# Kernel tuning notes

Hardware: AMD Instinct MI355X
Metric: run time of the kernel (lower is better)

Reference implementation:

```python
import jax, jax.numpy as jnp
import numpy as np

BN_EPS = 1e-5


def gcn_conv(x, src, dst, W, b):
    # PyG GCNConv: add self-loops, symmetric normalization, bias after aggregation
    n = x.shape[0]
    h = x @ W                                   # [N, d]
    deg = jnp.zeros((n,), x.dtype).at[dst].add(1.0) + 1.0  # in-degree + self-loop
    dinv = jax.lax.rsqrt(deg)
    norm = dinv[src] * dinv[dst]                # [E]
    agg = jnp.zeros_like(h).at[dst].add(h[src] * norm[:, None])
    agg = agg + h * (dinv * dinv)[:, None]      # self-loop messages
    return agg + b


def batchnorm(x, gamma, beta):
    mu = x.mean(0)
    var = x.var(0)  # biased, as torch BN training mode
    return (x - mu) * jax.lax.rsqrt(var + BN_EPS) * gamma + beta


def mha(x, w_in, b_in, w_out, b_out, n_heads=4):
    # torch nn.MultiheadAttention, input [L, N, E]
    L, N, d = x.shape
    hd = d // n_heads
    qkv = x @ w_in.T + b_in                     # [L, N, 3d]
    q, k, v = jnp.split(qkv, 3, axis=-1)
    rh = lambda t: t.reshape(L, N, n_heads, hd)
    q = rh(q) * (1.0 / np.sqrt(hd))
    k, v = rh(k), rh(v)
    scores = jnp.einsum('lnhd,mnhd->nhlm', q, k)
    a = jax.nn.softmax(scores, axis=-1)
    o = jnp.einsum('nhlm,mnhd->lnhd', a, v).reshape(L, N, d)
    return o @ w_out.T + b_out


def setup_inputs() -> dict:
    key = jax.random.key(0)
    N, d, E, L, R = 50000, 128, 400000, 3, 4
    ks = jax.random.split(key, 12)
    s = 1.0 / np.sqrt(d)
    return {
        'features': jax.random.normal(ks[0], (N, d), jnp.float32),
        'rel_emb': jax.random.normal(ks[1], (R, d), jnp.float32),
        'edge_index': jax.random.randint(ks[2], (R, 2, E), 0, N, dtype=jnp.int32),
        'W_gcn': jax.random.normal(ks[3], (L, d, d), jnp.float32) * s,
        'b_gcn': jnp.zeros((L, d), jnp.float32),
        'bn_gamma': jnp.ones((L - 1, d), jnp.float32),
        'bn_beta': jnp.zeros((L - 1, d), jnp.float32),
        'W_rt': jax.random.normal(ks[4], (L, d, d), jnp.float32) * s,
        'b_rt': jnp.zeros((L, d), jnp.float32),
        'attn_w_in': jax.random.normal(ks[5], (3 * d, d), jnp.float32) * s,
        'attn_b_in': jnp.zeros((3 * d,), jnp.float32),
        'attn_w_out': jax.random.normal(ks[6], (d, d), jnp.float32) * s,
        'attn_b_out': jnp.zeros((d,), jnp.float32),
        'alphas': jnp.full((4,), 0.95, jnp.float32),
        'fusion_q': jax.random.normal(ks[7], (d,), jnp.float32),
        'fusion_w': jax.random.normal(ks[8], (d, d), jnp.float32) * s,
        'fusion_b': jnp.zeros((d,), jnp.float32),
    }


def reference(features, rel_emb, edge_index, W_gcn, b_gcn, bn_gamma, bn_beta,
              W_rt, b_rt, attn_w_in, attn_b_in, attn_w_out, attn_b_out,
              alphas, fusion_q, fusion_w, fusion_b):
    L = W_gcn.shape[0]
    # RelationGCN unpacks rel_emb as (poi_r, s_r, d_r, n_r) and processes
    # relations in order (n, poi, s, d) -> permute to processing order.
    perm = jnp.array([3, 0, 1, 2])
    rels = rel_emb[perm]                # [4, d], order (n, poi, s, d)
    edges = edge_index[perm]            # [4, 2, E]
    embs = jnp.broadcast_to(features, (4,) + features.shape)  # all start at features

    def inner(emb, r, src, dst, Wg, bg, gamma, beta):
        h = gcn_conv(emb * r, src, dst, Wg, bg)
        return emb + jax.nn.leaky_relu(batchnorm(h, gamma, beta))

    for i in range(L - 1):
        embs = jax.vmap(inner, in_axes=(0, 0, 0, 0, None, None, None, None))(
            embs, rels, edges[:, 0], edges[:, 1],
            W_gcn[i], b_gcn[i], bn_gamma[i], bn_beta[i])
        rels = rels @ W_rt[i].T + b_rt[i]
        # dropout p=0.0 -> identity

    embs = jax.vmap(lambda e, r, s_, t_: gcn_conv(e * r, s_, t_, W_gcn[-1], b_gcn[-1]))(
        embs, rels, edges[:, 0], edges[:, 1])
    rels = rels @ W_rt[-1].T + b_rt[-1]

    # PM_Model mis-unpacks RelationGCN outputs (returned order n,poi,s,d as
    # poi,s,d,n). CrossLayer then stacks (n_emb, poi_emb, d_emb, s_emb) which in
    # true processing order is (d, n, s, poi):
    stk = jnp.stack([embs[3], embs[0], embs[2], embs[1]])  # [4, N, d]
    fusion = mha(stk, attn_w_in, attn_b_in, attn_w_out, attn_b_out)
    a = alphas  # [alpha_n, alpha_poi, alpha_d, alpha_s]
    n_f = fusion[0] * a[0] + (1 - a[0]) * stk[0]
    poi_f = fusion[1] * a[1] + (1 - a[1]) * stk[1]
    d_f = fusion[2] * a[2] + (1 - a[2]) * stk[2]
    s_f = fusion[3] * a[3] + (1 - a[3]) * stk[3]

    def score(f):
        return jnp.mean(jnp.sum(jax.nn.leaky_relu(f @ fusion_w.T + fusion_b) * fusion_q, axis=1))

    w = jax.nn.softmax(jnp.stack([score(n_f), score(poi_f), score(s_f), score(d_f)]))
    region = w[0] * n_f + w[1] * poi_f + w[2] * s_f + w[3] * d_f

    # Final multiplies use the same mis-unpacked rel names:
    # n_r<-rels[3](true d), poi_r<-rels[0](true n), s_r<-rels[1], d_r<-rels[2]
    return (region, region * rels[3], region * rels[0], region * rels[1], region * rels[2])
```

## Files before the change

### kernel.cpp

```cpp
#include <hip/hip_runtime.h>
#include <cstdio>

#define DD 128
#define NREL 4

using short8 = __attribute__((ext_vector_type(8))) short;
using f32x4  = __attribute__((ext_vector_type(4))) float;

struct PtrB4 { const unsigned short* p[4]; };
struct OutB4 { unsigned short* p[4]; };

__device__ __forceinline__ int edge_perm(int r) { return (r + 3) & 3; }

__device__ __forceinline__ float bf_lo(unsigned u) { return __uint_as_float(u << 16); }
__device__ __forceinline__ float bf_hi(unsigned u) { return __uint_as_float(u & 0xffff0000u); }
__device__ __forceinline__ float bfe(short s) {
  return __uint_as_float(((unsigned)(unsigned short)s) << 16);
}
__device__ __forceinline__ unsigned short f2bf(float f) {
  unsigned x = __float_as_uint(f);
  unsigned r = (x + 0x7fffu + ((x >> 16) & 1u)) >> 16;
  return (unsigned short)r;
}
__device__ __forceinline__ unsigned pack2(float a, float b) {
  return (unsigned)f2bf(a) | ((unsigned)f2bf(b) << 16);
}


__global__ void rels_init(const float* __restrict__ rel_emb, float* __restrict__ rels) {
  int t = threadIdx.x;
  int r = t >> 7, c = t & 127;
  rels[t] = rel_emb[edge_perm(r) * DD + c];
}

__global__ void rels_update(const float* __restrict__ rin, const float* __restrict__ Wrt,
                            const float* __restrict__ brt, float* __restrict__ rout) {
  int t = threadIdx.x;
  int r = t >> 7, j = t & 127;
  float s = brt[j];
  const float* wr = Wrt + j * DD;
  const float* xr = rin + r * DD;
  for (int c = 0; c < DD; ++c) s += xr[c] * wr[c];
  rout[t] = s;
}

__global__ void scale_w_bf(const float* __restrict__ rels_i, const float* __restrict__ Wg,
                           unsigned short* __restrict__ Wsb) {
  int i = blockIdx.x * 256 + threadIdx.x;
  int r = i >> 14, rem = i & 16383, j = rem >> 7, c = rem & 127;
  Wsb[i] = f2bf(rels_i[r * DD + c] * Wg[c * DD + j]);
}

__global__ void conv_w(const float* __restrict__ w_in, const float* __restrict__ w_out,
                       const float* __restrict__ w_fus, unsigned short* __restrict__ Wab) {
  int i = blockIdx.x * 256 + threadIdx.x;
  float v = (i < 49152) ? w_in[i] : (i < 65536 ? w_out[i - 49152] : w_fus[i - 65536]);
  Wab[i] = f2bf(v);
}

__global__ void conv_f2b(const float* __restrict__ in, unsigned* __restrict__ out2, size_t n4) {
  size_t i = (size_t)blockIdx.x * 256 + threadIdx.x;
  if (i < n4) {
    float4 v = ((const float4*)in)[i];
    out2[i * 2]     = pack2(v.x, v.y);
    out2[i * 2 + 1] = pack2(v.z, v.w);
  }
}


__global__ void count_deg(const int* __restrict__ ei, int* __restrict__ deg, int N, int E) {
  int r = blockIdx.y;
  int base = blockIdx.x * 1024 + threadIdx.x;
  const int* dsts = ei + (size_t)edge_perm(r) * 2 * E + E;
#pragma unroll
  for (int k = 0; k < 4; ++k) {
    int e = base + k * 256;
    if (e < E) atomicAdd(deg + (size_t)r * N + dsts[e], 1);
  }
}

__global__ void finalize_dinv(const int* __restrict__ deg, float* __restrict__ dinv, int total) {
  int i = blockIdx.x * 256 + threadIdx.x;
  if (i < total) dinv[i] = rsqrtf((float)deg[i] + 1.0f);
}

__global__ void scan_block(const int* __restrict__ deg, int* __restrict__ excl,
                           int* __restrict__ bsums, int n) {
  __shared__ int sh[256];
  int i = blockIdx.x * 256 + threadIdx.x;
  int v = (i < n) ? deg[i] : 0;
  sh[threadIdx.x] = v;
  __syncthreads();
  for (int st = 1; st < 256; st <<= 1) {
    int t = (threadIdx.x >= st) ? sh[threadIdx.x - st] : 0;
    __syncthreads();
    sh[threadIdx.x] += t;
    __syncthreads();
  }
  if (i < n) excl[i] = sh[threadIdx.x] - v;
  if (threadIdx.x == 255) bsums[blockIdx.x] = sh[255];
}

__global__ void scan_sums(int* __restrict__ bsums, int nb) {
  __shared__ int sh[1024];
  int v = (threadIdx.x < nb) ? bsums[threadIdx.x] : 0;
  sh[threadIdx.x] = v;
  __syncthreads();
  for (int st = 1; st < 1024; st <<= 1) {
    int t = (threadIdx.x >= st) ? sh[threadIdx.x - st] : 0;
    __syncthreads();
    sh[threadIdx.x] += t;
    __syncthreads();
  }
  if (threadIdx.x < nb) bsums[threadIdx.x] = sh[threadIdx.x] - v;
}

__global__ void scan_add(int* __restrict__ excl, int* __restrict__ cursor,
                         const int* __restrict__ bsums, int n) {
  int i = blockIdx.x * 256 + threadIdx.x;
  if (i < n) {
    int o = excl[i] + bsums[blockIdx.x];
    excl[i] = o;
    cursor[i] = o;
  }
}

__global__ void fill_edges(const int* __restrict__ ei, int* __restrict__ cursor,
                           int* __restrict__ srcbuf, int N, int E) {
  int r = blockIdx.y;
  int base = blockIdx.x * 1024 + threadIdx.x;
  const int* bp = ei + (size_t)edge_perm(r) * 2 * E;
  int s[4], d[4], pos[4];
#pragma unroll
  for (int k = 0; k < 4; ++k) {
    int e = base + k * 256;
    s[k] = (e < E) ? bp[e] : 0;
    d[k] = (e < E) ? bp[E + e] : 0;
  }
#pragma unroll
  for (int k = 0; k < 4; ++k) {
    int e = base + k * 256;
    if (e < E) pos[k] = atomicAdd(&cursor[r * N + d[k]], 1);
  }
#pragma unroll
  for (int k = 0; k < 4; ++k) {
    int e = base + k * 256;
    if (e < E) srcbuf[pos[k]] = r * N + s[k];
  }
}

template <int MODE>
__global__ __launch_bounds__(256) void gemm_ws(PtrB4 xs, PtrB4 wz, OutB4 ys,
                                               const float* __restrict__ bias,
                                               const float* __restrict__ dinv, int M) {
  int z = blockIdx.y;
  const unsigned short* __restrict__ X = xs.p[z];
  const unsigned short* __restrict__ W = wz.p[z];
  int tid = threadIdx.x;
  int wave = tid >> 6, lane = tid & 63;
  int r16 = lane & 15, kgrp = lane >> 4;
  int rowhalf = wave >> 1, colbase = (wave & 1) * 64;
  int blockrow = blockIdx.x * 64;

  short8 b[4][4];
#pragma unroll
  for (int s = 0; s < 4; ++s)
#pragma unroll
    for (int cn = 0; cn < 4; ++cn)
      b[s][cn] = *(const short8*)(W + ((colbase + cn * 16 + r16) << 7) + s * 32 + kgrp * 8);

  int row0 = blockrow + rowhalf * 32 + r16;
  int r0c = row0 < M ? row0 : M - 1;
  int r1c = row0 + 16 < M ? row0 + 16 : M - 1;
  short8 a[2][4];
#pragma unroll
  for (int s = 0; s < 4; ++s) {
    a[0][s] = *(const short8*)(X + (size_t)r0c * DD + s * 32 + kgrp * 8);
    a[1][s] = *(const short8*)(X + (size_t)r1c * DD + s * 32 + kgrp * 8);
  }

  f32x4 acc[2][4];
#pragma unroll
  for (int rt = 0; rt < 2; ++rt)
#pragma unroll
    for (int cn = 0; cn < 4; ++cn)
#pragma unroll
      for (int j = 0; j < 4; ++j) acc[rt][cn][j] = 0.f;

#pragma unroll
  for (int s = 0; s < 4; ++s)
#pragma unroll
    for (int rt = 0; rt < 2; ++rt)
#pragma unroll
      for (int cn = 0; cn < 4; ++cn)
        acc[rt][cn] = __builtin_amdgcn_mfma_f32_16x16x32_bf16(a[rt][s], b[s][cn], acc[rt][cn], 0, 0, 0);

  __shared__ __align__(16) unsigned short tile[64][DD + 8];
  float dv[2][4];
  if constexpr (MODE == 0) {
#pragma unroll
    for (int rt = 0; rt < 2; ++rt)
#pragma unroll
      for (int i = 0; i < 4; ++i) {
        int row = blockrow + rowhalf * 32 + rt * 16 + kgrp * 4 + i;
        dv[rt][i] = dinv[(size_t)z * M + (row < M ? row : 0)];
      }
  }
#pragma unroll
  for (int rt = 0; rt < 2; ++rt)
#pragma unroll
    for (int cn = 0; cn < 4; ++cn) {
      int col = colbase + cn * 16 + r16;
#pragma unroll
      for (int i = 0; i < 4; ++i) {
        int wrow = rowhalf * 32 + rt * 16 + kgrp * 4 + i;
        float y = acc[rt][cn][i];
        if constexpr (MODE == 0) y *= dv[rt][i];
        tile[wrow][col] = f2bf(y);
      }
    }
  __syncthreads();
  int orow = tid >> 2, seg = tid & 3;
  int grow = blockrow + orow;
  if (grow < M) {
    unsigned short* Yp = ys.p[z] + (size_t)grow * DD + seg * 32;
    const unsigned short* tp = &tile[orow][seg * 32];
#pragma unroll
    for (int k = 0; k < 4; ++k)
      *(uint4*)(Yp + k * 8) = *(const uint4*)(tp + k * 8);
  }
}

template <int WB>
__global__ __launch_bounds__(256) void gemm_upd(PtrB4 res, PtrB4 abs_, PtrB4 wz,
                                                OutB4 xout, OutB4 ys,
                                                const float* __restrict__ ssx,
                                                const float* __restrict__ dinv, int M) {
  int z = blockIdx.y;
  const unsigned short* __restrict__ R = res.p[z];
  const unsigned short* __restrict__ A = abs_.p[z];
  const unsigned short* __restrict__ W = wz.p[z];
  int tid = threadIdx.x;

  __shared__ float ssc[DD], ssh[DD];
  if (tid < DD) {
    ssc[tid] = ssx[((size_t)z * DD + tid) * 2];
    ssh[tid] = ssx[((size_t)z * DD + tid) * 2 + 1];
  }
  __syncthreads();

  int wave = tid >> 6, lane = tid & 63;
  int r16 = lane & 15, kgrp = lane >> 4;
  int rowhalf = wave >> 1, colbase = (wave & 1) * 64;
  int blockrow = blockIdx.x * 64;

  short8 b[4][4];
#pragma unroll
  for (int s = 0; s < 4; ++s)
#pragma unroll
    for (int cn = 0; cn < 4; ++cn)
      b[s][cn] = *(const short8*)(W + ((colbase + cn * 16 + r16) << 7) + s * 32 + kgrp * 8);

  int row0 = blockrow + rowhalf * 32 + r16;
  int rc[2];
  rc[0] = row0 < M ? row0 : M - 1;
  rc[1] = row0 + 16 < M ? row0 + 16 : M - 1;
  short8 a[2][4];
#pragma unroll
  for (int rt = 0; rt < 2; ++rt)
#pragma unroll
    for (int s = 0; s < 4; ++s) {
      int cbase = s * 32 + kgrp * 8;
      short8 rv = *(const short8*)(R + (size_t)rc[rt] * DD + cbase);
      short8 av = *(const short8*)(A + (size_t)rc[rt] * DD + cbase);
      short8 av2;
#pragma unroll
      for (int j = 0; j < 8; ++j) {
        float x = bfe(av[j]) * ssc[cbase + j] + ssh[cbase + j];
        x = x > 0.f ? x : 0.01f * x;
        av2[j] = (short)f2bf(bfe(rv[j]) + x);
      }
      a[rt][s] = av2;
    }
  if (WB) {
#pragma unroll
    for (int rt = 0; rt < 2; ++rt) {
      int row = row0 + rt * 16;
      if (row < M) {
#pragma unroll
        for (int s = 0; s < 4; ++s)
          *(short8*)(xout.p[z] + (size_t)row * DD + s * 32 + kgrp * 8) = a[rt][s];
      }
    }
  }

  f32x4 acc[2][4];
#pragma unroll
  for (int rt = 0; rt < 2; ++rt)
#pragma unroll
    for (int cn = 0; cn < 4; ++cn)
#pragma unroll
      for (int j = 0; j < 4; ++j) acc[rt][cn][j] = 0.f;
#pragma unroll
  for (int s = 0; s < 4; ++s)
#pragma unroll
    for (int rt = 0; rt < 2; ++rt)
#pragma unroll
      for (int cn = 0; cn < 4; ++cn)
        acc[rt][cn] = __builtin_amdgcn_mfma_f32_16x16x32_bf16(a[rt][s], b[s][cn], acc[rt][cn], 0, 0, 0);

  __shared__ __align__(16) unsigned short tile[64][DD + 8];
  float dv[2][4];
#pragma unroll
  for (int rt = 0; rt < 2; ++rt)
#pragma unroll
    for (int i = 0; i < 4; ++i) {
      int row = blockrow + rowhalf * 32 + rt * 16 + kgrp * 4 + i;
      dv[rt][i] = dinv[(size_t)z * M + (row < M ? row : 0)];
    }
#pragma unroll
  for (int rt = 0; rt < 2; ++rt)
#pragma unroll
    for (int cn = 0; cn < 4; ++cn) {
      int col = colbase + cn * 16 + r16;
#pragma unroll
      for (int i = 0; i < 4; ++i) {
        int wrow = rowhalf * 32 + rt * 16 + kgrp * 4 + i;
        tile[wrow][col] = f2bf(acc[rt][cn][i] * dv[rt][i]);
      }
    }
  __syncthreads();
  int orow = tid >> 2, seg = tid & 3;
  int grow = blockrow + orow;
  if (grow < M) {
    unsigned short* Yp = ys.p[z] + (size_t)grow * DD + seg * 32;
    const unsigned short* tp = &tile[orow][seg * 32];
#pragma unroll
    for (int k = 0; k < 4; ++k)
      *(uint4*)(Yp + k * 8) = *(const uint4*)(tp + k * 8);
  }
}

__global__ __launch_bounds__(256) void attn_mega(PtrB4 stks,
    const unsigned short* __restrict__ Wab,
    const float* __restrict__ b_in, const float* __restrict__ b_out,
    const float* __restrict__ alphas, const float* __restrict__ fus_b,
    const float* __restrict__ fq, unsigned short* __restrict__ fbuf,
    float* __restrict__ S, int N) {
  __shared__ __align__(16) unsigned short q_s[64][136];
  __shared__ __align__(16) unsigned short k_s[64][136];
  __shared__ __align__(16) unsigned short v_s[64][136];
  __shared__ float ps[16][64];
  __shared__ float lred[4];
  size_t NK = (size_t)N * DD;

  int tid = threadIdx.x;
  int wave = tid >> 6, lane = tid & 63;
  int r16 = lane & 15, kgrp = lane >> 4;
  int rowhalf = wave >> 1, colbase = (wave & 1) * 64;
  int nodebase = blockIdx.x * 16;

  int rlo = rowhalf * 32 + r16;
  int rhi = rlo + 16;
  int nlo = nodebase + (rlo & 15); if (nlo >= N) nlo = N - 1;
  int nhi = nodebase + (rhi & 15); if (nhi >= N) nhi = N - 1;
  const unsigned short* a0p = stks.p[rlo >> 4] + (size_t)nlo * DD + kgrp * 8;
  const unsigned short* a1p = stks.p[rhi >> 4] + (size_t)nhi * DD + kgrp * 8;
  short8 A0[4], A1[4];
#pragma unroll
  for (int s = 0; s < 4; ++s) {
    A0[s] = *(const short8*)(a0p + s * 32);
    A1[s] = *(const short8*)(a1p + s * 32);
  }

  for (int o = 0; o < 3; ++o) {
    const unsigned short* W = Wab + o * 16384;
    short8 b[4][4];
#pragma unroll
    for (int s = 0; s < 4; ++s)
#pragma unroll
      for (int cn = 0; cn < 4; ++cn)
        b[s][cn] = *(const short8*)(W + ((colbase + cn * 16 + r16) << 7) + s * 32 + kgrp * 8);
    f32x4 acc[2][4];
#pragma unroll
    for (int rt = 0; rt < 2; ++rt)
#pragma unroll
      for (int cn = 0; cn < 4; ++cn)
#pragma unroll
        for (int j = 0; j < 4; ++j) acc[rt][cn][j] = 0.f;
#pragma unroll
    for (int s = 0; s < 4; ++s)
#pragma unroll
      for (int cn = 0; cn < 4; ++cn) {
        acc[0][cn] = __builtin_amdgcn_mfma_f32_16x16x32_bf16(A0[s], b[s][cn], acc[0][cn], 0, 0, 0);
        acc[1][cn] = __builtin_amdgcn_mfma_f32_16x16x32_bf16(A1[s], b[s][cn], acc[1][cn], 0, 0, 0);
      }
    unsigned short (*dst)[136] = (o == 0) ? q_s : (o == 1) ? k_s : v_s;
#pragma unroll
    for (int rt = 0; rt < 2; ++rt)
#pragma unroll
      for (int cn = 0; cn < 4; ++cn) {
        int col = colbase + cn * 16 + r16;
        float bb = b_in[o * DD + col];
#pragma unroll
        for (int i = 0; i < 4; ++i) {
          int wrow = rowhalf * 32 + rt * 16 + kgrp * 4 + i;
          dst[wrow][col] = f2bf(acc[rt][cn][i] + bb);
        }
      }
  }
  __syncthreads();

  {
    int h = lane >> 4, li = (lane >> 2) & 3, m = lane & 3;
    int c0 = lane * 2, hh = c0 >> 5;
    for (int t = 0; t < 4; ++t) {
      int nd = wave * 4 + t;
      float sc = 0.f;
#pragma unroll
      for (int s4 = 0; s4 < 4; ++s4) {
        short8 qv = *(const short8*)&q_s[li * 16 + nd][h * 32 + s4 * 8];
        short8 kv = *(const short8*)&k_s[m * 16 + nd][h * 32 + s4 * 8];
#pragma unroll
        for (int j = 0; j < 8; ++j) sc += bfe(qv[j]) * bfe(kv[j]);
      }
      sc *= 0.17677669529663687f;
      float mx = sc;
      mx = fmaxf(mx, __shfl_xor(mx, 1));
      mx = fmaxf(mx, __shfl_xor(mx, 2));
      float e = expf(sc - mx);
      float sum = e;
      sum += __shfl_xor(sum, 1);
      sum += __shfl_xor(sum, 2);
      ps[nd][lane] = e / sum;
      unsigned v0 = *(const unsigned*)&v_s[0 * 16 + nd][c0];
      unsigned v1 = *(const unsigned*)&v_s[1 * 16 + nd][c0];
      unsigned v2 = *(const unsigned*)&v_s[2 * 16 + nd][c0];
      unsigned v3 = *(const unsigned*)&v_s[3 * 16 + nd][c0];
      float vl[4] = {bf_lo(v0), bf_lo(v1), bf_lo(v2), bf_lo(v3)};
      float vh[4] = {bf_hi(v0), bf_hi(v1), bf_hi(v2), bf_hi(v3)};
#pragma unroll
      for (int lo = 0; lo < 4; ++lo) {
        const float* pp = &ps[nd][hh * 16 + lo * 4];
        float ol = pp[0] * vl[0] + pp[1] * vl[1] + pp[2] * vl[2] + pp[3] * vl[3];
        float oh = pp[0] * vh[0] + pp[1] * vh[1] + pp[2] * vh[2] + pp[3] * vh[3];
        *(unsigned*)&q_s[lo * 16 + nd][c0] = pack2(ol, oh);
      }
    }
  }
  __syncthreads();

  {
    const unsigned short* W = Wab + 3 * 16384;
    short8 b[4][4];
#pragma unroll
    for (int s = 0; s < 4; ++s)
#pragma unroll
      for (int cn = 0; cn < 4; ++cn)
        b[s][cn] = *(const short8*)(W + ((colbase + cn * 16 + r16) << 7) + s * 32 + kgrp * 8);
    short8 AO0[4], AO1[4];
#pragma unroll
    for (int s = 0; s < 4; ++s) {
      AO0[s] = *(const short8*)&q_s[rlo][s * 32 + kgrp * 8];
      AO1[s] = *(const short8*)&q_s[rhi][s * 32 + kgrp * 8];
    }
    f32x4 acc[2][4];
#pragma unroll
    for (int rt = 0; rt < 2; ++rt)
#pragma unroll
      for (int cn = 0; cn < 4; ++cn)
#pragma unroll
        for (int j = 0; j < 4; ++j) acc[rt][cn][j] = 0.f;
#pragma unroll
    for (int s = 0; s < 4; ++s)
#pragma unroll
      for (int cn = 0; cn < 4; ++cn) {
        acc[0][cn] = __builtin_amdgcn_mfma_f32_16x16x32_bf16(AO0[s], b[s][cn], acc[0][cn], 0, 0, 0);
        acc[1][cn] = __builtin_amdgcn_mfma_f32_16x16x32_bf16(AO1[s], b[s][cn], acc[1][cn], 0, 0, 0);
      }
    __syncthreads();
#pragma unroll
    for (int rt = 0; rt < 2; ++rt)
#pragma unroll
      for (int cn = 0; cn < 4; ++cn) {
        int col = colbase + cn * 16 + r16;
        float bb = b_out[col];
#pragma unroll
        for (int i = 0; i < 4; ++i) {
          int wrow = rowhalf * 32 + rt * 16 + kgrp * 4 + i;
          k_s[wrow][col] = f2bf(acc[rt][cn][i] + bb);
        }
      }
  }
  __syncthreads();

  {
    int orow = tid >> 2, seg = tid & 3;
    int lb = orow >> 4, nb = nodebase + (orow & 15);
    if (nb < N) {
      float aa = alphas[lb], na = 1.f - aa;
      const unsigned short* sp = stks.p[lb] + (size_t)nb * DD + seg * 32;
      unsigned short* tp = &k_s[orow][seg * 32];
      unsigned short* Yp = fbuf + (size_t)lb * NK + (size_t)nb * DD + seg * 32;
#pragma unroll
      for (int k = 0; k < 4; ++k) {
        uint4 pv = *(const uint4*)(tp + k * 8);
        uint4 sv = *(const uint4*)(sp + k * 8);
        const unsigned* pw = &pv.x;
        const unsigned* sw = &sv.x;
        uint4 o; unsigned* ow = &o.x;
#pragma unroll
        for (int j = 0; j < 4; ++j)
          ow[j] = pack2(aa * bf_lo(pw[j]) + na * bf_lo(sw[j]),
                        aa * bf_hi(pw[j]) + na * bf_hi(sw[j]));
        *(uint4*)(Yp + k * 8) = o;
        *(uint4*)(tp + k * 8) = o;
      }
    }
  }
  __syncthreads();

  {
    const unsigned short* W = Wab + 4 * 16384;
    short8 b[4][4];
#pragma unroll
    for (int s = 0; s < 4; ++s)
#pragma unroll
      for (int cn = 0; cn < 4; ++cn)
        b[s][cn] = *(const short8*)(W + ((colbase + cn * 16 + r16) << 7) + s * 32 + kgrp * 8);
    short8 AF0[4], AF1[4];
#pragma unroll
    for (int s = 0; s < 4; ++s) {
      AF0[s] = *(const short8*)&k_s[rlo][s * 32 + kgrp * 8];
      AF1[s] = *(const short8*)&k_s[rhi][s * 32 + kgrp * 8];
    }
    f32x4 acc[2][4];
#pragma unroll
    for (int rt = 0; rt < 2; ++rt)
#pragma unroll
      for (int cn = 0; cn < 4; ++cn)
#pragma unroll
        for (int j = 0; j < 4; ++j) acc[rt][cn][j] = 0.f;
#pragma unroll
    for (int s = 0; s < 4; ++s)
#pragma unroll
      for (int cn = 0; cn < 4; ++cn) {
        acc[0][cn] = __builtin_amdgcn_mfma_f32_16x16x32_bf16(AF0[s], b[s][cn], acc[0][cn], 0, 0, 0);
        acc[1][cn] = __builtin_amdgcn_mfma_f32_16x16x32_bf16(AF1[s], b[s][cn], acc[1][cn], 0, 0, 0);
      }
    float ss0 = 0.f, ss1 = 0.f;
#pragma unroll
    for (int cn = 0; cn < 4; ++cn) {
      int col = colbase + cn * 16 + r16;
      float bb = fus_b[col];
      float qc = fq[col];
#pragma unroll
      for (int i = 0; i < 4; ++i) {
        if (nodebase + kgrp * 4 + i < N) {
          float y0 = acc[0][cn][i] + bb;
          float y1 = acc[1][cn][i] + bb;
          ss0 += (y0 > 0.f ? y0 : 0.01f * y0) * qc;
          ss1 += (y1 > 0.f ? y1 : 0.01f * y1) * qc;
        }
      }
    }
    if (tid < 4) lred[tid] = 0.f;
    __syncthreads();
    atomicAdd(&lred[rowhalf * 2], ss0);
    atomicAdd(&lred[rowhalf * 2 + 1], ss1);
    __syncthreads();
    if (tid < 4) atomicAdd(S + tid, lred[tid]);
  }
}

__global__ __launch_bounds__(256) void gather_agg(const int* __restrict__ srcbuf,
                                                  const int* __restrict__ offs,
                                                  const int* __restrict__ deg,
                                                  const float* __restrict__ dinv,
                                                  const uint2* __restrict__ Bs2,
                                                  const float* __restrict__ bias,
                                                  uint2* __restrict__ Ab2, int N4) {
  int rn = blockIdx.x * 8 + (threadIdx.x >> 5);
  if (rn >= N4) return;
  int lane = threadIdx.x & 31;
  int st = offs[rn], cnt = deg[rn];
  uint2 u = Bs2[(size_t)rn * 32 + lane];
  float a0 = bf_lo(u.x), a1 = bf_hi(u.x), a2 = bf_lo(u.y), a3 = bf_hi(u.y);
  int e = 0;
  for (; e + 8 <= cnt; e += 8) {
    int rr[8];
#pragma unroll
    for (int j = 0; j < 8; ++j) rr[j] = srcbuf[st + e + j];
    uint2 vv[8];
#pragma unroll
    for (int j = 0; j < 8; ++j) vv[j] = Bs2[(size_t)rr[j] * 32 + lane];
#pragma unroll
    for (int j = 0; j < 8; ++j) {
      a0 += bf_lo(vv[j].x); a1 += bf_hi(vv[j].x);
      a2 += bf_lo(vv[j].y); a3 += bf_hi(vv[j].y);
    }
  }
  if (e + 4 <= cnt) {
    int rr[4];
#pragma unroll
    for (int j = 0; j < 4; ++j) rr[j] = srcbuf[st + e + j];
    uint2 vv[4];
#pragma unroll
    for (int j = 0; j < 4; ++j) vv[j] = Bs2[(size_t)rr[j] * 32 + lane];
#pragma unroll
    for (int j = 0; j < 4; ++j) {
      a0 += bf_lo(vv[j].x); a1 += bf_hi(vv[j].x);
      a2 += bf_lo(vv[j].y); a3 += bf_hi(vv[j].y);
    }
    e += 4;
  }
  for (; e < cnt; ++e) {
    uint2 v = Bs2[(size_t)srcbuf[st + e] * 32 + lane];
    a0 += bf_lo(v.x); a1 += bf_hi(v.x); a2 += bf_lo(v.y); a3 += bf_hi(v.y);
  }
  float dvv = dinv[rn];
  int c = lane * 4;
  uint2 o;
  o.x = pack2(a0 * dvv + bias[c],     a1 * dvv + bias[c + 1]);
  o.y = pack2(a2 * dvv + bias[c + 2], a3 * dvv + bias[c + 3]);
  Ab2[(size_t)rn * 32 + lane] = o;
}


__global__ void bn_stats(const unsigned* __restrict__ Ab2, float* __restrict__ sums, int N) {
  int r = blockIdx.y;
  int lane = threadIdx.x & 63, grp = threadIdx.x >> 6;
  float s0 = 0.f, q0 = 0.f, s1 = 0.f, q1 = 0.f;
  const unsigned* base = Ab2 + (size_t)r * N * 64;
  for (int n = blockIdx.x * 4 + grp; n < N; n += gridDim.x * 4) {
    unsigned u = base[(size_t)n * 64 + lane];
    float a = bf_lo(u), b = bf_hi(u);
    s0 += a; q0 += a * a; s1 += b; q1 += b * b;
  }
  __shared__ float sh[4][64][4];
  sh[grp][lane][0] = s0; sh[grp][lane][1] = q0; sh[grp][lane][2] = s1; sh[grp][lane][3] = q1;
  __syncthreads();
  if (grp == 0) {
#pragma unroll
    for (int g = 1; g < 4; ++g) {
      s0 += sh[g][lane][0]; q0 += sh[g][lane][1]; s1 += sh[g][lane][2]; q1 += sh[g][lane][3];
    }
    int c0 = lane * 2;
    atomicAdd(sums + (r * DD + c0) * 2, s0);
    atomicAdd(sums + (r * DD + c0) * 2 + 1, q0);
    atomicAdd(sums + (r * DD + c0 + 1) * 2, s1);
    atomicAdd(sums + (r * DD + c0 + 1) * 2 + 1, q1);
  }
}

__global__ void bn_final(const float* __restrict__ sums, const float* __restrict__ gamma,
                         const float* __restrict__ beta, float* __restrict__ ss, int N) {
  int t = threadIdx.x;
  int c = t & 127;
  float mu = sums[t * 2] / N;
  float var = sums[t * 2 + 1] / N - mu * mu;
  float sc = gamma[c] * rsqrtf(var + 1e-5f);
  ss[t * 2] = sc;
  ss[t * 2 + 1] = beta[c] - mu * sc;
}

__global__ void wcoef(const float* __restrict__ S, float* __restrict__ coef, int N) {
  if (threadIdx.x == 0) {
    float v0 = S[0] / N, v1 = S[1] / N, v2 = S[3] / N, v3 = S[2] / N;
    float mx = fmaxf(fmaxf(v0, v1), fmaxf(v2, v3));
    float e0 = expf(v0 - mx), e1 = expf(v1 - mx), e2 = expf(v2 - mx), e3 = expf(v3 - mx);
    float inv = 1.f / (e0 + e1 + e2 + e3);
    coef[0] = e0 * inv; coef[1] = e1 * inv; coef[2] = e3 * inv; coef[3] = e2 * inv;
  }
}

__device__ __forceinline__ float bfat(uint2 u, int j) {
  unsigned w = (j < 2) ? u.x : u.y;
  return (j & 1) ? bf_hi(w) : bf_lo(w);
}

__global__ void final_out(const unsigned short* __restrict__ fb, const float* __restrict__ coef,
                          const float* __restrict__ rels3, float* __restrict__ out, int N) {
  size_t NK = (size_t)N * DD;
  size_t i4 = (size_t)blockIdx.x * 256 + threadIdx.x;
  if (i4 >= NK / 4) return;
  size_t g = i4 * 4;
  int c = (int)(g & 127);
  float c0 = coef[0], c1 = coef[1], c2 = coef[2], c3 = coef[3];
  uint2 u0 = *(const uint2*)(fb + g);
  uint2 u1 = *(const uint2*)(fb + NK + g);
  uint2 u2 = *(const uint2*)(fb + 2 * NK + g);
  uint2 u3 = *(const uint2*)(fb + 3 * NK + g);
  float4 reg4, o1, o2, o3, o4;
  float* rp = &reg4.x; float* p1 = &o1.x; float* p2 = &o2.x; float* p3 = &o3.x; float* p4 = &o4.x;
#pragma unroll
  for (int j = 0; j < 4; ++j) {
    float region = c0 * bfat(u0, j) + c1 * bfat(u1, j) + c2 * bfat(u2, j) + c3 * bfat(u3, j);
    rp[j] = region;
    p1[j] = region * rels3[3 * DD + c + j];
    p2[j] = region * rels3[0 * DD + c + j];
    p3[j] = region * rels3[1 * DD + c + j];
    p4[j] = region * rels3[2 * DD + c + j];
  }
  *(float4*)(out + g) = reg4;
  *(float4*)(out + NK + g) = o1;
  *(float4*)(out + 2 * NK + g) = o2;
  *(float4*)(out + 3 * NK + g) = o3;
  *(float4*)(out + 4 * NK + g) = o4;
}


extern "C" void kernel_launch(void* const* d_in, const int* in_sizes, int n_in,
                              void* d_out, int out_size, void* d_ws, size_t ws_size,
                              hipStream_t stream) {
  const float* features  = (const float*)d_in[0];
  const float* rel_emb   = (const float*)d_in[1];
  const int*   edge_idx  = (const int*)d_in[2];
  const float* W_gcn     = (const float*)d_in[3];
  const float* b_gcn     = (const float*)d_in[4];
  const float* bn_gamma  = (const float*)d_in[5];
  const float* bn_beta   = (const float*)d_in[6];
  const float* W_rt      = (const float*)d_in[7];
  const float* b_rt      = (const float*)d_in[8];
  const float* attn_w_in = (const float*)d_in[9];
  const float* attn_b_in = (const float*)d_in[10];
  const float* attn_wout = (const float*)d_in[11];
  const float* attn_bout = (const float*)d_in[12];
  const float* alphas    = (const float*)d_in[13];
  const float* fusion_q  = (const float*)d_in[14];
  const float* fusion_w  = (const float*)d_in[15];
  const float* fusion_b  = (const float*)d_in[16];

  int N = in_sizes[0] / DD;
  int E = in_sizes[2] / (2 * NREL);
  size_t NK = (size_t)N * DD;
  int N4 = 4 * N;

  unsigned short* Xb = (unsigned short*)d_ws;
  unsigned short* Bs = Xb + 4 * NK;
  unsigned short* Ab = Bs + 4 * NK;
  unsigned short* Ub = Ab + 4 * NK;
  unsigned short* Fb = Ub + 4 * NK;
  float* dinv  = (float*)(Fb + NK);
  unsigned short* Wgcnb = (unsigned short*)(dinv + N4);
  unsigned short* Wab   = Wgcnb + 4 * DD * DD;
  float* rels  = (float*)(Wab + 5 * DD * DD);
  float* bnsum = rels + 4 * 512;
  float* bnss  = bnsum + 1024;
  float* S     = bnss + 1024;
  float* coef  = S + 4;
  int* deg_i   = (int*)(coef + 4);
  int* offs    = deg_i + N4;
  int* cur     = offs + N4;
  int* bsums   = cur + N4;
  int* srcb    = bsums + 1024;

  size_t needed = (size_t)((char*)(srcb + 4 * E) - (char*)d_ws);
  if (ws_size < needed) {
    fprintf(stderr, "kernel_launch: ws too small (%zu < %zu)\n", ws_size, needed);
    return;
  }

  int gemmGrid = (N + 63) / 64;
  int scanBlocks = (N4 + 255) / 256;
  int egrid4 = (E + 1023) / 1024;

  hipMemsetAsync(deg_i, 0, (size_t)N4 * sizeof(int), stream);
  count_deg<<<dim3(egrid4, 4), 256, 0, stream>>>(edge_idx, deg_i, N, E);
  finalize_dinv<<<scanBlocks, 256, 0, stream>>>(deg_i, dinv, N4);
  scan_block<<<scanBlocks, 256, 0, stream>>>(deg_i, offs, bsums, N4);
  scan_sums<<<1, 1024, 0, stream>>>(bsums, scanBlocks);
  scan_add<<<scanBlocks, 256, 0, stream>>>(offs, cur, bsums, N4);
  fill_edges<<<dim3(egrid4, 4), 256, 0, stream>>>(edge_idx, cur, srcb, N, E);

  rels_init<<<1, 512, 0, stream>>>(rel_emb, rels);
  conv_w<<<5 * 16384 / 256, 256, 0, stream>>>(attn_w_in, attn_wout, fusion_w, Wab);
  conv_f2b<<<(int)((NK / 4 + 255) / 256), 256, 0, stream>>>(features, (unsigned*)Fb, NK / 4);

  PtrB4 wz, abIn, resIn;
  OutB4 msgOut, xbOut, dummyO;
  for (int r = 0; r < 4; ++r) {
    wz.p[r] = Wgcnb + (size_t)r * DD * DD;
    abIn.p[r] = Ab + (size_t)r * NK;
    msgOut.p[r] = Bs + (size_t)r * NK;
    xbOut.p[r] = Xb + (size_t)r * NK;
    dummyO.p[r] = nullptr;
  }

  scale_w_bf<<<256, 256, 0, stream>>>(rels, W_gcn, Wgcnb);
  {
    PtrB4 xs; for (int r = 0; r < 4; ++r) xs.p[r] = Fb;
    gemm_ws<0><<<dim3(gemmGrid, 4), 256, 0, stream>>>(xs, wz, msgOut, nullptr, dinv, N);
  }
  gather_agg<<<(N4 + 7) / 8, 256, 0, stream>>>(srcb, offs, deg_i, dinv, (const uint2*)Bs,
                                               b_gcn, (uint2*)Ab, N4);
  hipMemsetAsync(bnsum, 0, 1024 * sizeof(float), stream);
  bn_stats<<<dim3(400, 4), 256, 0, stream>>>((const unsigned*)Ab, bnsum, N);
  bn_final<<<1, 512, 0, stream>>>(bnsum, bn_gamma, bn_beta, bnss, N);
  rels_update<<<1, 512, 0, stream>>>(rels, W_rt, b_rt, rels + 512);

  scale_w_bf<<<256, 256, 0, stream>>>(rels + 512, W_gcn + (size_t)DD * DD, Wgcnb);
  for (int r = 0; r < 4; ++r) resIn.p[r] = Fb;
  gemm_upd<1><<<dim3(gemmGrid, 4), 256, 0, stream>>>(resIn, abIn, wz, xbOut, msgOut,
                                                     bnss, dinv, N);
  gather_agg<<<(N4 + 7) / 8, 256, 0, stream>>>(srcb, offs, deg_i, dinv, (const uint2*)Bs,
                                               b_gcn + DD, (uint2*)Ab, N4);
  hipMemsetAsync(bnsum, 0, 1024 * sizeof(float), stream);
  bn_stats<<<dim3(400, 4), 256, 0, stream>>>((const unsigned*)Ab, bnsum, N);
  bn_final<<<1, 512, 0, stream>>>(bnsum, bn_gamma + DD, bn_beta + DD, bnss, N);
  rels_update<<<1, 512, 0, stream>>>(rels + 512, W_rt + (size_t)DD * DD, b_rt + DD, rels + 1024);

  scale_w_bf<<<256, 256, 0, stream>>>(rels + 1024, W_gcn + (size_t)2 * DD * DD, Wgcnb);
  for (int r = 0; r < 4; ++r) resIn.p[r] = Xb + (size_t)r * NK;
  gemm_upd<0><<<dim3(gemmGrid, 4), 256, 0, stream>>>(resIn, abIn, wz, dummyO, msgOut,
                                                     bnss, dinv, N);
  gather_agg<<<(N4 + 7) / 8, 256, 0, stream>>>(srcb, offs, deg_i, dinv, (const uint2*)Bs,
                                               b_gcn + 2 * DD, (uint2*)Ab, N4);
  rels_update<<<1, 512, 0, stream>>>(rels + 1024, W_rt + (size_t)2 * DD * DD, b_rt + 2 * DD,
                                     rels + 1536);

  const int pstk[4] = {3, 0, 2, 1};
  PtrB4 stk;
  for (int l = 0; l < 4; ++l) stk.p[l] = Ab + (size_t)pstk[l] * NK;

  hipMemsetAsync(S, 0, 4 * sizeof(float), stream);
  attn_mega<<<(N + 15) / 16, 256, 0, stream>>>(stk, Wab, attn_b_in, attn_bout, alphas,
                                               fusion_b, fusion_q, Bs, S, N);
  wcoef<<<1, 64, 0, stream>>>(S, coef, N);
  final_out<<<(int)((NK / 4 + 255) / 256), 256, 0, stream>>>(Bs, coef, rels + 1536,
                                                             (float*)d_out, N);
}
```

Before: 962.5 us.

## Cut attn_mega LDS footprint with swizzled two-buffer layout and shuffle-based probabilities

The fused attention kernel drops the separate V and probability shared buffers. V is computed after softmax into the reused Q buffer, and probabilities stay in registers, shared across lanes with __shfl. An XOR swizzle on the column index reduces LDS bank conflicts, and launch bounds now request 4 blocks per SM, aiming for higher occupancy. The cost is an extra barrier plus shuffles in the P·V loop, and register pressure is tighter under the new launch bound.

```diff
diff --git a/kernel.cpp b/kernel.cpp
--- a/kernel.cpp
+++ b/kernel.cpp
@@ -25,6 +25,8 @@
 __device__ __forceinline__ unsigned pack2(float a, float b) {
   return (unsigned)f2bf(a) | ((unsigned)f2bf(b) << 16);
 }
+
+#define SWIDX(row, col) ((row) * 136 + ((col) ^ ((((row) >> 4) & 3) << 4)))
 
 
 __global__ void rels_init(const float* __restrict__ rel_emb, float* __restrict__ rels) {
@@ -341,16 +343,14 @@
   }
 }
 
-__global__ __launch_bounds__(256) void attn_mega(PtrB4 stks,
+__global__ __launch_bounds__(256, 4) void attn_mega(PtrB4 stks,
     const unsigned short* __restrict__ Wab,
     const float* __restrict__ b_in, const float* __restrict__ b_out,
     const float* __restrict__ alphas, const float* __restrict__ fus_b,
     const float* __restrict__ fq, unsigned short* __restrict__ fbuf,
     float* __restrict__ S, int N) {
-  __shared__ __align__(16) unsigned short q_s[64][136];
-  __shared__ __align__(16) unsigned short k_s[64][136];
-  __shared__ __align__(16) unsigned short v_s[64][136];
-  __shared__ float ps[16][64];
+  __shared__ __align__(16) unsigned short q_s[64 * 136];
+  __shared__ __align__(16) unsigned short k_s[64 * 136];
   __shared__ float lred[4];
   size_t NK = (size_t)N * DD;
 
@@ -373,7 +373,7 @@
     A1[s] = *(const short8*)(a1p + s * 32);
   }
 
-  for (int o = 0; o < 3; ++o) {
+  for (int o = 0; o < 2; ++o) {
     const unsigned short* W = Wab + o * 16384;
     short8 b[4][4];
 #pragma unroll
@@ -395,7 +395,7 @@
         acc[0][cn] = __builtin_amdgcn_mfma_f32_16x16x32_bf16(A0[s], b[s][cn], acc[0][cn], 0, 0, 0);
         acc[1][cn] = __builtin_amdgcn_mfma_f32_16x16x32_bf16(A1[s], b[s][cn], acc[1][cn], 0, 0, 0);
       }
-    unsigned short (*dst)[136] = (o == 0) ? q_s : (o == 1) ? k_s : v_s;
+    unsigned short* dst = (o == 0) ? q_s : k_s;
 #pragma unroll
     for (int rt = 0; rt < 2; ++rt)
 #pragma unroll
@@ -405,22 +405,22 @@
 #pragma unroll
         for (int i = 0; i < 4; ++i) {
           int wrow = rowhalf * 32 + rt * 16 + kgrp * 4 + i;
-          dst[wrow][col] = f2bf(acc[rt][cn][i] + bb);
+          dst[SWIDX(wrow, col)] = f2bf(acc[rt][cn][i] + bb);
         }
       }
   }
   __syncthreads();
 
+  float p[4];
   {
     int h = lane >> 4, li = (lane >> 2) & 3, m = lane & 3;
-    int c0 = lane * 2, hh = c0 >> 5;
     for (int t = 0; t < 4; ++t) {
       int nd = wave * 4 + t;
       float sc = 0.f;
 #pragma unroll
       for (int s4 = 0; s4 < 4; ++s4) {
-        short8 qv = *(const short8*)&q_s[li * 16 + nd][h * 32 + s4 * 8];
-        short8 kv = *(const short8*)&k_s[m * 16 + nd][h * 32 + s4 * 8];
+        short8 qv = *(const short8*)&q_s[SWIDX(li * 16 + nd, h * 32 + s4 * 8)];
+        short8 kv = *(const short8*)&k_s[SWIDX(m * 16 + nd, h * 32 + s4 * 8)];
 #pragma unroll
         for (int j = 0; j < 8; ++j) sc += bfe(qv[j]) * bfe(kv[j]);
       }
@@ -432,19 +432,66 @@
       float sum = e;
       sum += __shfl_xor(sum, 1);
       sum += __shfl_xor(sum, 2);
-      ps[nd][lane] = e / sum;
-      unsigned v0 = *(const unsigned*)&v_s[0 * 16 + nd][c0];
-      unsigned v1 = *(const unsigned*)&v_s[1 * 16 + nd][c0];
-      unsigned v2 = *(const unsigned*)&v_s[2 * 16 + nd][c0];
-      unsigned v3 = *(const unsigned*)&v_s[3 * 16 + nd][c0];
-      float vl[4] = {bf_lo(v0), bf_lo(v1), bf_lo(v2), bf_lo(v3)};
-      float vh[4] = {bf_hi(v0), bf_hi(v1), bf_hi(v2), bf_hi(v3)};
+      p[t] = e / sum;
+    }
+  }
+  __syncthreads();
+
+  {
+    const unsigned short* W = Wab + 2 * 16384;
+    short8 b[4][4];
+#pragma unroll
+    for (int s = 0; s < 4; ++s)
+#pragma unroll
+      for (int cn = 0; cn < 4; ++cn)
+        b[s][cn] = *(const short8*)(W + ((colbase + cn * 16 + r16) << 7) + s * 32 + kgrp * 8);
+    f32x4 acc[2][4];
+#pragma unroll
+    for (int rt = 0; rt < 2; ++rt)
+#pragma unroll
+      for (int cn = 0; cn < 4; ++cn)
+#pragma unroll
+        for (int j = 0; j < 4; ++j) acc[rt][cn][j] = 0.f;
+#pragma unroll
+    for (int s = 0; s < 4; ++s)
+#pragma unroll
+      for (int cn = 0; cn < 4; ++cn) {
+        acc[0][cn] = __builtin_amdgcn_mfma_f32_16x16x32_bf16(A0[s], b[s][cn], acc[0][cn], 0, 0, 0);
+        acc[1][cn] = __builtin_amdgcn_mfma_f32_16x16x32_bf16(A1[s], b[s][cn], acc[1][cn], 0, 0, 0);
+      }
+#pragma unroll
+    for (int rt = 0; rt < 2; ++rt)
+#pragma unroll
+      for (int cn = 0; cn < 4; ++cn) {
+        int col = colbase + cn * 16 + r16;
+        float bb = b_in[2 * DD + col];
+#pragma unroll
+        for (int i = 0; i < 4; ++i) {
+          int wrow = rowhalf * 32 + rt * 16 + kgrp * 4 + i;
+          q_s[SWIDX(wrow, col)] = f2bf(acc[rt][cn][i] + bb);
+        }
+      }
+  }
+  __syncthreads();
+
+  {
+    int c0 = lane * 2, hh = lane >> 4;
+    for (int t = 0; t < 4; ++t) {
+      int nd = wave * 4 + t;
+      unsigned v[4];
+#pragma unroll
+      for (int m = 0; m < 4; ++m)
+        v[m] = *(const unsigned*)&q_s[SWIDX(m * 16 + nd, c0)];
 #pragma unroll
       for (int lo = 0; lo < 4; ++lo) {
-        const float* pp = &ps[nd][hh * 16 + lo * 4];
-        float ol = pp[0] * vl[0] + pp[1] * vl[1] + pp[2] * vl[2] + pp[3] * vl[3];
-        float oh = pp[0] * vh[0] + pp[1] * vh[1] + pp[2] * vh[2] + pp[3] * vh[3];
-        *(unsigned*)&q_s[lo * 16 + nd][c0] = pack2(ol, oh);
+        float ol = 0.f, oh = 0.f;
+#pragma unroll
+        for (int m = 0; m < 4; ++m) {
+          float pm = __shfl(p[t], hh * 16 + lo * 4 + m);
+          ol += pm * bf_lo(v[m]);
+          oh += pm * bf_hi(v[m]);
+        }
+        *(unsigned*)&k_s[SWIDX(lo * 16 + nd, c0)] = pack2(ol, oh);
       }
     }
   }
@@ -461,8 +508,8 @@
     short8 AO0[4], AO1[4];
 #pragma unroll
     for (int s = 0; s < 4; ++s) {
-      AO0[s] = *(const short8*)&q_s[rlo][s * 32 + kgrp * 8];
-      AO1[s] = *(const short8*)&q_s[rhi][s * 32 + kgrp * 8];
+      AO0[s] = *(const short8*)&k_s[SWIDX(rlo, s * 32 + kgrp * 8)];
+      AO1[s] = *(const short8*)&k_s[SWIDX(rhi, s * 32 + kgrp * 8)];
     }
     f32x4 acc[2][4];
 #pragma unroll
@@ -478,7 +525,6 @@
         acc[0][cn] = __builtin_amdgcn_mfma_f32_16x16x32_bf16(AO0[s], b[s][cn], acc[0][cn], 0, 0, 0);
         acc[1][cn] = __builtin_amdgcn_mfma_f32_16x16x32_bf16(AO1[s], b[s][cn], acc[1][cn], 0, 0, 0);
       }
-    __syncthreads();
 #pragma unroll
     for (int rt = 0; rt < 2; ++rt)
 #pragma unroll
@@ -488,7 +534,7 @@
 #pragma unroll
         for (int i = 0; i < 4; ++i) {
           int wrow = rowhalf * 32 + rt * 16 + kgrp * 4 + i;
-          k_s[wrow][col] = f2bf(acc[rt][cn][i] + bb);
+          q_s[SWIDX(wrow, col)] = f2bf(acc[rt][cn][i] + bb);
         }
       }
   }
@@ -500,11 +546,11 @@
     if (nb < N) {
       float aa = alphas[lb], na = 1.f - aa;
       const unsigned short* sp = stks.p[lb] + (size_t)nb * DD + seg * 32;
-      unsigned short* tp = &k_s[orow][seg * 32];
       unsigned short* Yp = fbuf + (size_t)lb * NK + (size_t)nb * DD + seg * 32;
 #pragma unroll
       for (int k = 0; k < 4; ++k) {
-        uint4 pv = *(const uint4*)(tp + k * 8);
+        unsigned short* tp = &q_s[SWIDX(orow, seg * 32 + k * 8)];
+        uint4 pv = *(const uint4*)tp;
         uint4 sv = *(const uint4*)(sp + k * 8);
         const unsigned* pw = &pv.x;
         const unsigned* sw = &sv.x;
@@ -514,7 +560,7 @@
           ow[j] = pack2(aa * bf_lo(pw[j]) + na * bf_lo(sw[j]),
                         aa * bf_hi(pw[j]) + na * bf_hi(sw[j]));
         *(uint4*)(Yp + k * 8) = o;
-        *(uint4*)(tp + k * 8) = o;
+        *(uint4*)tp = o;
       }
     }
   }
@@ -531,8 +577,8 @@
     short8 AF0[4], AF1[4];
 #pragma unroll
     for (int s = 0; s < 4; ++s) {
-      AF0[s] = *(const short8*)&k_s[rlo][s * 32 + kgrp * 8];
-      AF1[s] = *(const short8*)&k_s[rhi][s * 32 + kgrp * 8];
+      AF0[s] = *(const short8*)&q_s[SWIDX(rlo, s * 32 + kgrp * 8)];
+      AF1[s] = *(const short8*)&q_s[SWIDX(rhi, s * 32 + kgrp * 8)];
     }
     f32x4 acc[2][4];
 #pragma unroll
```

Result: slower. 1.011 ms (+5.1%).
